# Kernel optimization log

Hardware: AMD Instinct MI355X
Metric: run time of the kernel (lower is better)

The kernel has to match this reference:

```python
import jax, jax.numpy as jnp
import numpy as np

B, KLEN, QLEN = 4, 512, 64
KDIM = QDIM = ADIM = 512
H = 4
DK = ADIM // H


def setup_inputs() -> dict:
    key = jax.random.key(0)
    ks = jax.random.split(key, 8)
    inp = {}
    inp["key"] = jax.random.normal(ks[0], (B, KLEN, KDIM), jnp.float32)
    inp["query"] = jax.random.normal(ks[1], (B, QLEN, QDIM), jnp.float32)
    inp["mask"] = jax.random.randint(ks[2], (B, QLEN, KLEN), 0, 2, jnp.int32)
    # nn.Linear default init scale ~ 1/sqrt(fan_in)
    inp["w_key_w"] = jax.random.normal(ks[3], (ADIM, KDIM), jnp.float32) / np.sqrt(KDIM)
    inp["w_key_b"] = jnp.zeros((ADIM,), jnp.float32)
    inp["w_query_w"] = jax.random.normal(ks[4], (ADIM, QDIM), jnp.float32) / np.sqrt(QDIM)
    # weight-normed v: weight = g * v / ||v||_row, g initialized to sqrt(1/adim)
    inp["v_v"] = jax.random.normal(ks[5], (H, ADIM), jnp.float32) / np.sqrt(ADIM)
    inp["v_g"] = jnp.full((H, 1), np.sqrt(1.0 / ADIM), jnp.float32)
    inp["r"] = jnp.array([-4.0], jnp.float32)  # init_r
    return inp


def reference(key, query, mask, w_key_w, w_key_b, w_query_w, v_v, v_g, r):
    bs, klen, _ = key.shape
    qlen = query.shape[1]
    # key projection -> [B, H, klen, d_k]
    k = (jnp.einsum('bkd,ad->bka', key, w_key_w) + w_key_b)
    k = k.reshape(bs, klen, H, DK).transpose(0, 2, 1, 3)
    # query projection (no bias) -> [B, H, qlen, d_k]
    q = jnp.einsum('bqd,ad->bqa', query, w_query_w)
    q = q.reshape(bs, qlen, H, DK).transpose(0, 2, 1, 3)
    # additive energy: relu(k + q) over [B, H, qlen, klen, d_k]
    e5 = jax.nn.relu(k[:, :, None, :, :] + q[:, :, :, None, :])
    # weight-normed v linear mixes heads: Wv[n, h, d]
    Wv = (v_g * v_v / jnp.linalg.norm(v_v, axis=1, keepdims=True)).reshape(H, H, DK)
    e = jnp.einsum('bhqkd,nhd->bnqk', e5, Wv)
    e = e + r[0]
    neg_inf = jnp.finfo(e.dtype).min
    m = jnp.broadcast_to(mask[:, None, :, :], e.shape)  # [B, H, qlen, klen]
    e = jnp.where(m == 0, neg_inf, e)
    return e
```

## Files before the change

### kernel.cpp

```cpp
#include <hip/hip_runtime.h>
#include <math.h>

#define KLEN 512
#define QLEN 64
#define ADIM 512
#define BATCH 4
#define NH 4

typedef __attribute__((ext_vector_type(8))) short bf16x8;
typedef __attribute__((ext_vector_type(4))) float f32x4;
typedef _Float16 f16;
typedef __attribute__((ext_vector_type(2))) _Float16 f16x2;

__device__ __forceinline__ unsigned short f2bf(float f) {
  unsigned int x = __float_as_uint(f);
  return (unsigned short)((x + 0x7FFFu + ((x >> 16) & 1u)) >> 16);
}
__device__ __forceinline__ f16x2 u2h(unsigned int u) {
  union { unsigned int u; f16x2 h; } v; v.u = u; return v.h;
}

__global__ __launch_bounds__(256) void proj_mfma(
    const float* __restrict__ key, const float* __restrict__ query,
    const float* __restrict__ wk, const float* __restrict__ bk,
    const float* __restrict__ wq,
    const float* __restrict__ v_v, const float* __restrict__ v_g,
    f16* __restrict__ Kp, f16* __restrict__ Qp, f16* __restrict__ Wn) {
  __shared__ short At[64 * 40];
  __shared__ short Wt[64 * 40];
  __shared__ float wred[256];

  const int bid = blockIdx.x;
  const int tid = threadIdx.x;

  if (bid == 288) {
    for (int h = 0; h < NH; ++h) {
      float v0 = v_v[h * ADIM + tid];
      float v1 = v_v[h * ADIM + tid + 256];
      wred[tid] = v0 * v0 + v1 * v1;
      __syncthreads();
      for (int s2 = 128; s2 > 0; s2 >>= 1) {
        if (tid < s2) wred[tid] += wred[tid + s2];
        __syncthreads();
      }
      float scale = v_g[h] / sqrtf(wred[0]);
      Wn[h * ADIM + tid] = (f16)(v0 * scale);
      Wn[h * ADIM + tid + 256] = (f16)(v1 * scale);
      __syncthreads();
    }
    return;
  }

  const float *A, *W, *bias;
  f16* C;
  int m0, a0;
  if (bid < 256) {
    A = key; W = wk; bias = bk; C = Kp;
    m0 = (bid >> 3) * 64; a0 = (bid & 7) * 64;
  } else {
    const int t = bid - 256;
    A = query; W = wq; bias = nullptr; C = Qp;
    m0 = (t >> 3) * 64; a0 = (t & 7) * 64;
  }

  const int wr = (tid >> 7) & 1;
  const int wc = (tid >> 6) & 1;
  const int lane = tid & 63;
  const int lr = lane & 15, hi = lane >> 4;

  const int r0 = tid >> 3, c0 = (tid & 7) * 4;
  const int r1 = (tid + 256) >> 3;

  f32x4 acc[2][2] = {};

  float4 fa0 = *(const float4*)&A[(size_t)(m0 + r0) * ADIM + c0];
  float4 fa1 = *(const float4*)&A[(size_t)(m0 + r1) * ADIM + c0];
  float4 fw0 = *(const float4*)&W[(size_t)(a0 + r0) * ADIM + c0];
  float4 fw1 = *(const float4*)&W[(size_t)(a0 + r1) * ADIM + c0];

  for (int c = 0; c < 16; ++c) {
    const int cn = ((c + 1) & 15) * 32;
    float4 na0 = *(const float4*)&A[(size_t)(m0 + r0) * ADIM + cn + c0];
    float4 na1 = *(const float4*)&A[(size_t)(m0 + r1) * ADIM + cn + c0];
    float4 nw0 = *(const float4*)&W[(size_t)(a0 + r0) * ADIM + cn + c0];
    float4 nw1 = *(const float4*)&W[(size_t)(a0 + r1) * ADIM + cn + c0];
    __syncthreads();
    short4 s;
    s = make_short4(f2bf(fa0.x), f2bf(fa0.y), f2bf(fa0.z), f2bf(fa0.w));
    *(short4*)&At[r0 * 40 + c0] = s;
    s = make_short4(f2bf(fa1.x), f2bf(fa1.y), f2bf(fa1.z), f2bf(fa1.w));
    *(short4*)&At[r1 * 40 + c0] = s;
    s = make_short4(f2bf(fw0.x), f2bf(fw0.y), f2bf(fw0.z), f2bf(fw0.w));
    *(short4*)&Wt[r0 * 40 + c0] = s;
    s = make_short4(f2bf(fw1.x), f2bf(fw1.y), f2bf(fw1.z), f2bf(fw1.w));
    *(short4*)&Wt[r1 * 40 + c0] = s;
    __syncthreads();
#pragma unroll
    for (int mi = 0; mi < 2; ++mi) {
      bf16x8 af = *(const bf16x8*)&At[(wr * 32 + mi * 16 + lr) * 40 + hi * 8];
#pragma unroll
      for (int ni = 0; ni < 2; ++ni) {
        bf16x8 wf = *(const bf16x8*)&Wt[(wc * 32 + ni * 16 + lr) * 40 + hi * 8];
        acc[mi][ni] = __builtin_amdgcn_mfma_f32_16x16x32_bf16(af, wf, acc[mi][ni], 0, 0, 0);
      }
    }
    fa0 = na0; fa1 = na1; fw0 = nw0; fw1 = nw1;
  }

#pragma unroll
  for (int ni = 0; ni < 2; ++ni) {
    const int ccol = a0 + wc * 32 + ni * 16 + lr;
    const float bv = bias ? bias[ccol] : 0.f;
#pragma unroll
    for (int mi = 0; mi < 2; ++mi)
#pragma unroll
      for (int i = 0; i < 4; ++i) {
        const int crow = m0 + wr * 32 + mi * 16 + hi * 4 + i;
        C[(size_t)crow * ADIM + ccol] = (f16)(acc[mi][ni][i] + bv);
      }
  }
}

__global__ __launch_bounds__(256) void energy_kernel(
    const f16* __restrict__ Kp, const f16* __restrict__ Qp,
    const f16* __restrict__ Wn, const int* __restrict__ mask,
    const float* __restrict__ r, float* __restrict__ out) {
  __shared__ f16 Kl[16 * 520];
  __shared__ f16 Ql[16 * 520];
  __shared__ f16 Wl[4 * 520];
  __shared__ float Red[2][1280];

  const int b = blockIdx.z;
  const int q0 = blockIdx.y * 16;
  const int kl0 = blockIdx.x * 16;
  const int tid = threadIdx.x;
  const int wave = tid >> 6;
  const int lane = tid & 63;
  const int klg = lane & 7;
  const int qg = lane >> 3;

  const float rv = r[0];

  const unsigned short* Kb = (const unsigned short*)(Kp + ((size_t)b * KLEN + kl0) * ADIM);
  const unsigned short* Qb = (const unsigned short*)(Qp + ((size_t)b * QLEN + q0) * ADIM);

#pragma unroll
  for (int j = 0; j < 4; ++j) {
    const int u = tid + 256 * j;
    const int row = u >> 6, c8 = (u & 63) * 8;
    *(uint4*)&Kl[row * 520 + c8] = *(const uint4*)&Kb[row * ADIM + c8];
    *(uint4*)&Ql[row * 520 + c8] = *(const uint4*)&Qb[row * ADIM + c8];
  }
  {
    const int row = tid >> 6, c8 = (tid & 63) * 8;
    *(uint4*)&Wl[row * 520 + c8] =
        *(const uint4*)&((const unsigned short*)Wn)[row * ADIM + c8];
  }
  __syncthreads();

  float acc[2][2][4] = {};
  const int abase = wave * 128;

#pragma unroll
  for (int s = 0; s < 16; ++s) {
    const int off = abase + s * 8;
    uint4 ka = *(const uint4*)&Kl[klg * 520 + off];
    uint4 kb = *(const uint4*)&Kl[(klg + 8) * 520 + off];
    uint4 qa = *(const uint4*)&Ql[qg * 520 + off];
    uint4 qb = *(const uint4*)&Ql[(qg + 8) * 520 + off];
    uint4 w0 = *(const uint4*)&Wl[0 * 520 + off];
    uint4 w1 = *(const uint4*)&Wl[1 * 520 + off];
    uint4 w2 = *(const uint4*)&Wl[2 * 520 + off];
    uint4 w3 = *(const uint4*)&Wl[3 * 520 + off];
    unsigned ks[2][4] = {{ka.x, ka.y, ka.z, ka.w}, {kb.x, kb.y, kb.z, kb.w}};
    unsigned qs[2][4] = {{qa.x, qa.y, qa.z, qa.w}, {qb.x, qb.y, qb.z, qb.w}};
    unsigned ws[4][4] = {{w0.x, w0.y, w0.z, w0.w}, {w1.x, w1.y, w1.z, w1.w},
                         {w2.x, w2.y, w2.z, w2.w}, {w3.x, w3.y, w3.z, w3.w}};
#pragma unroll
    for (int j = 0; j < 4; ++j) {
      const f16x2 wv0 = u2h(ws[0][j]), wv1 = u2h(ws[1][j]);
      const f16x2 wv2 = u2h(ws[2][j]), wv3 = u2h(ws[3][j]);
#pragma unroll
      for (int ki = 0; ki < 2; ++ki) {
        const f16x2 kv = u2h(ks[ki][j]);
#pragma unroll
        for (int qi = 0; qi < 2; ++qi) {
          f16x2 sum = kv + u2h(qs[qi][j]);
          f16x2 rl = __builtin_elementwise_max(sum, (f16x2)(_Float16)0);
          acc[ki][qi][0] = __builtin_amdgcn_fdot2(rl, wv0, acc[ki][qi][0], false);
          acc[ki][qi][1] = __builtin_amdgcn_fdot2(rl, wv1, acc[ki][qi][1], false);
          acc[ki][qi][2] = __builtin_amdgcn_fdot2(rl, wv2, acc[ki][qi][2], false);
          acc[ki][qi][3] = __builtin_amdgcn_fdot2(rl, wv3, acc[ki][qi][3], false);
        }
      }
    }
  }

  const int half = wave & 1;
  if (wave < 2) {
#pragma unroll
    for (int ki = 0; ki < 2; ++ki)
#pragma unroll
      for (int qi = 0; qi < 2; ++qi) {
        const int cell = (qg + 8 * qi) * 16 + klg + 8 * ki;
#pragma unroll
        for (int n = 0; n < 4; ++n) Red[half][cell * 5 + n] = acc[ki][qi][n];
      }
  }
  __syncthreads();
  if (wave >= 2) {
#pragma unroll
    for (int ki = 0; ki < 2; ++ki)
#pragma unroll
      for (int qi = 0; qi < 2; ++qi) {
        const int cell = (qg + 8 * qi) * 16 + klg + 8 * ki;
#pragma unroll
        for (int n = 0; n < 4; ++n) Red[half][cell * 5 + n] += acc[ki][qi][n];
      }
  }
  __syncthreads();

  const float NEG_BIG = __uint_as_float(0xFF7F0000u);
  const int n = tid >> 6;
  const int q = (tid >> 2) & 15;
  const int klb = (tid & 3) * 4;
  const int4 mv = *(const int4*)&mask[((size_t)b * QLEN + q0 + q) * KLEN + kl0 + klb];
  const int mm[4] = {mv.x, mv.y, mv.z, mv.w};
  float4 o;
  float* op = &o.x;
#pragma unroll
  for (int t = 0; t < 4; ++t) {
    const int cell = q * 16 + klb + t;
    float v = Red[0][cell * 5 + n] + Red[1][cell * 5 + n] + rv;
    op[t] = mm[t] ? v : NEG_BIG;
  }
  *(float4*)&out[(((size_t)b * NH + n) * QLEN + q0 + q) * KLEN + kl0 + klb] = o;
}

extern "C" void kernel_launch(void* const* d_in, const int* in_sizes, int n_in,
                              void* d_out, int out_size, void* d_ws, size_t ws_size,
                              hipStream_t stream) {
  const float* key   = (const float*)d_in[0];
  const float* query = (const float*)d_in[1];
  const int*   mask  = (const int*)d_in[2];
  const float* wk    = (const float*)d_in[3];
  const float* bk    = (const float*)d_in[4];
  const float* wq    = (const float*)d_in[5];
  const float* v_v   = (const float*)d_in[6];
  const float* v_g   = (const float*)d_in[7];
  const float* r     = (const float*)d_in[8];
  float* out = (float*)d_out;

  f16* Kp = (f16*)d_ws;
  f16* Qp = Kp + (size_t)2048 * 512;
  f16* Wn = Qp + (size_t)256 * 512;

  hipLaunchKernelGGL(proj_mfma, dim3(289), dim3(256), 0, stream,
                     key, query, wk, bk, wq, v_v, v_g, Kp, Qp, Wn);
  hipLaunchKernelGGL(energy_kernel, dim3(32, 4, 4), dim3(256), 0, stream,
                     Kp, Qp, Wn, mask, r, out);
}
```

Before: 24.54 us.

## Load MFMA operands directly from global and read Wn via scalar loads

The projection GEMM drops its LDS staging and barriers. Each lane now loads its MFMA fragment straight from global memory, and the bf16 conversion changes from round-to-nearest to plain truncation via byte permute. In the energy kernel the Wn tile is no longer staged in LDS. Its reads use a wave-uniform offset (readfirstlane) so the compiler can issue scalar loads, which cuts LDS traffic and frees LDS space. The costs are uncoalesced, strided global loads in the GEMM with no reuse across waves, and slightly less accurate bf16 rounding.

```diff
diff --git a/kernel.cpp b/kernel.cpp
--- a/kernel.cpp
+++ b/kernel.cpp
@@ -12,12 +12,17 @@
 typedef _Float16 f16;
 typedef __attribute__((ext_vector_type(2))) _Float16 f16x2;
 
-__device__ __forceinline__ unsigned short f2bf(float f) {
-  unsigned int x = __float_as_uint(f);
-  return (unsigned short)((x + 0x7FFFu + ((x >> 16) & 1u)) >> 16);
-}
 __device__ __forceinline__ f16x2 u2h(unsigned int u) {
   union { unsigned int u; f16x2 h; } v; v.u = u; return v.h;
+}
+
+__device__ __forceinline__ bf16x8 pack8(float4 x, float4 y) {
+  union { unsigned int u[4]; bf16x8 v; } o;
+  o.u[0] = __builtin_amdgcn_perm(__float_as_uint(x.y), __float_as_uint(x.x), 0x07060302);
+  o.u[1] = __builtin_amdgcn_perm(__float_as_uint(x.w), __float_as_uint(x.z), 0x07060302);
+  o.u[2] = __builtin_amdgcn_perm(__float_as_uint(y.y), __float_as_uint(y.x), 0x07060302);
+  o.u[3] = __builtin_amdgcn_perm(__float_as_uint(y.w), __float_as_uint(y.z), 0x07060302);
+  return o.v;
 }
 
 __global__ __launch_bounds__(256) void proj_mfma(
@@ -26,14 +31,11 @@
     const float* __restrict__ wq,
     const float* __restrict__ v_v, const float* __restrict__ v_g,
     f16* __restrict__ Kp, f16* __restrict__ Qp, f16* __restrict__ Wn) {
-  __shared__ short At[64 * 40];
-  __shared__ short Wt[64 * 40];
-  __shared__ float wred[256];
-
   const int bid = blockIdx.x;
   const int tid = threadIdx.x;
 
   if (bid == 288) {
+    __shared__ float wred[256];
     for (int h = 0; h < NH; ++h) {
       float v0 = v_v[h * ADIM + tid];
       float v1 = v_v[h * ADIM + tid + 256];
@@ -68,43 +70,32 @@
   const int lane = tid & 63;
   const int lr = lane & 15, hi = lane >> 4;
 
-  const int r0 = tid >> 3, c0 = (tid & 7) * 4;
-  const int r1 = (tid + 256) >> 3;
+  const float* Ar0 = &A[(size_t)(m0 + wr * 32 + lr) * ADIM];
+  const float* Ar1 = Ar0 + 16 * ADIM;
+  const float* Br0 = &W[(size_t)(a0 + wc * 32 + lr) * ADIM];
+  const float* Br1 = Br0 + 16 * ADIM;
 
   f32x4 acc[2][2] = {};
 
-  float4 fa0 = *(const float4*)&A[(size_t)(m0 + r0) * ADIM + c0];
-  float4 fa1 = *(const float4*)&A[(size_t)(m0 + r1) * ADIM + c0];
-  float4 fw0 = *(const float4*)&W[(size_t)(a0 + r0) * ADIM + c0];
-  float4 fw1 = *(const float4*)&W[(size_t)(a0 + r1) * ADIM + c0];
-
+#pragma unroll
   for (int c = 0; c < 16; ++c) {
-    const int cn = ((c + 1) & 15) * 32;
-    float4 na0 = *(const float4*)&A[(size_t)(m0 + r0) * ADIM + cn + c0];
-    float4 na1 = *(const float4*)&A[(size_t)(m0 + r1) * ADIM + cn + c0];
-    float4 nw0 = *(const float4*)&W[(size_t)(a0 + r0) * ADIM + cn + c0];
-    float4 nw1 = *(const float4*)&W[(size_t)(a0 + r1) * ADIM + cn + c0];
-    __syncthreads();
-    short4 s;
-    s = make_short4(f2bf(fa0.x), f2bf(fa0.y), f2bf(fa0.z), f2bf(fa0.w));
-    *(short4*)&At[r0 * 40 + c0] = s;
-    s = make_short4(f2bf(fa1.x), f2bf(fa1.y), f2bf(fa1.z), f2bf(fa1.w));
-    *(short4*)&At[r1 * 40 + c0] = s;
-    s = make_short4(f2bf(fw0.x), f2bf(fw0.y), f2bf(fw0.z), f2bf(fw0.w));
-    *(short4*)&Wt[r0 * 40 + c0] = s;
-    s = make_short4(f2bf(fw1.x), f2bf(fw1.y), f2bf(fw1.z), f2bf(fw1.w));
-    *(short4*)&Wt[r1 * 40 + c0] = s;
-    __syncthreads();
-#pragma unroll
-    for (int mi = 0; mi < 2; ++mi) {
-      bf16x8 af = *(const bf16x8*)&At[(wr * 32 + mi * 16 + lr) * 40 + hi * 8];
-#pragma unroll
-      for (int ni = 0; ni < 2; ++ni) {
-        bf16x8 wf = *(const bf16x8*)&Wt[(wc * 32 + ni * 16 + lr) * 40 + hi * 8];
-        acc[mi][ni] = __builtin_amdgcn_mfma_f32_16x16x32_bf16(af, wf, acc[mi][ni], 0, 0, 0);
-      }
-    }
-    fa0 = na0; fa1 = na1; fw0 = nw0; fw1 = nw1;
+    const int col = c * 32 + hi * 8;
+    float4 xa0 = *(const float4*)&Ar0[col];
+    float4 ya0 = *(const float4*)&Ar0[col + 4];
+    float4 xa1 = *(const float4*)&Ar1[col];
+    float4 ya1 = *(const float4*)&Ar1[col + 4];
+    float4 xb0 = *(const float4*)&Br0[col];
+    float4 yb0 = *(const float4*)&Br0[col + 4];
+    float4 xb1 = *(const float4*)&Br1[col];
+    float4 yb1 = *(const float4*)&Br1[col + 4];
+    bf16x8 fa0 = pack8(xa0, ya0);
+    bf16x8 fa1 = pack8(xa1, ya1);
+    bf16x8 fb0 = pack8(xb0, yb0);
+    bf16x8 fb1 = pack8(xb1, yb1);
+    acc[0][0] = __builtin_amdgcn_mfma_f32_16x16x32_bf16(fa0, fb0, acc[0][0], 0, 0, 0);
+    acc[0][1] = __builtin_amdgcn_mfma_f32_16x16x32_bf16(fa0, fb1, acc[0][1], 0, 0, 0);
+    acc[1][0] = __builtin_amdgcn_mfma_f32_16x16x32_bf16(fa1, fb0, acc[1][0], 0, 0, 0);
+    acc[1][1] = __builtin_amdgcn_mfma_f32_16x16x32_bf16(fa1, fb1, acc[1][1], 0, 0, 0);
   }
 
 #pragma unroll
@@ -127,7 +118,6 @@
     const float* __restrict__ r, float* __restrict__ out) {
   __shared__ f16 Kl[16 * 520];
   __shared__ f16 Ql[16 * 520];
-  __shared__ f16 Wl[4 * 520];
   __shared__ float Red[2][1280];
 
   const int b = blockIdx.z;
@@ -151,15 +141,12 @@
     *(uint4*)&Kl[row * 520 + c8] = *(const uint4*)&Kb[row * ADIM + c8];
     *(uint4*)&Ql[row * 520 + c8] = *(const uint4*)&Qb[row * ADIM + c8];
   }
-  {
-    const int row = tid >> 6, c8 = (tid & 63) * 8;
-    *(uint4*)&Wl[row * 520 + c8] =
-        *(const uint4*)&((const unsigned short*)Wn)[row * ADIM + c8];
-  }
   __syncthreads();
 
   float acc[2][2][4] = {};
-  const int abase = wave * 128;
+  const int uwave = __builtin_amdgcn_readfirstlane(wave);
+  const int abase = uwave * 128;
+  const unsigned int* Wd = (const unsigned int*)Wn;
 
 #pragma unroll
   for (int s = 0; s < 16; ++s) {
@@ -168,10 +155,10 @@
     uint4 kb = *(const uint4*)&Kl[(klg + 8) * 520 + off];
     uint4 qa = *(const uint4*)&Ql[qg * 520 + off];
     uint4 qb = *(const uint4*)&Ql[(qg + 8) * 520 + off];
-    uint4 w0 = *(const uint4*)&Wl[0 * 520 + off];
-    uint4 w1 = *(const uint4*)&Wl[1 * 520 + off];
-    uint4 w2 = *(const uint4*)&Wl[2 * 520 + off];
-    uint4 w3 = *(const uint4*)&Wl[3 * 520 + off];
+    uint4 w0 = *(const uint4*)&Wd[0 * 256 + (off >> 1)];
+    uint4 w1 = *(const uint4*)&Wd[1 * 256 + (off >> 1)];
+    uint4 w2 = *(const uint4*)&Wd[2 * 256 + (off >> 1)];
+    uint4 w3 = *(const uint4*)&Wd[3 * 256 + (off >> 1)];
     unsigned ks[2][4] = {{ka.x, ka.y, ka.z, ka.w}, {kb.x, kb.y, kb.z, kb.w}};
     unsigned qs[2][4] = {{qa.x, qa.y, qa.z, qa.w}, {qb.x, qb.y, qb.z, qb.w}};
     unsigned ws[4][4] = {{w0.x, w0.y, w0.z, w0.w}, {w1.x, w1.y, w1.z, w1.w},
```

Result: slower. 45.02 us (+83.4%).
